# Optimization experiments

Measured on AMD Instinct MI355X. Metric: run time of the kernel, lower is better.

Reference implementation:

```python
import jax, jax.numpy as jnp
import numpy as np

B, F, H, W, C = 1, 16, 32, 32, 128


def setup_inputs() -> dict:
    key = jax.random.key(0)
    ks = jax.random.split(key, 6)
    w = lambda k: jax.random.normal(k, (C, C), jnp.float32) * 0.02
    return {
        "x": jax.random.normal(ks[0], (B, F, H, W, C), jnp.float32),
        "gamma": jnp.ones((C,), jnp.float32),
        "wq": w(ks[1]), "bq": jnp.zeros((C,), jnp.float32),
        "wk": w(ks[2]), "bk": jnp.zeros((C,), jnp.float32),
        "wv": w(ks[3]), "bv": jnp.zeros((C,), jnp.float32),
        "wo": w(ks[4]), "bo": jnp.zeros((C,), jnp.float32),
    }


def reference(x, gamma, wq, bq, wk, bk, wv, bv, wo, bo):
    b, f, h, w_, c = x.shape
    s, n_hw = f * h * w_, h * w_
    identity = x

    # RMSNorm variant: L2-normalize over channels, rescale by sqrt(C) * gamma
    xn = x / (jnp.linalg.norm(x, axis=-1, keepdims=True) + 1e-8)
    xn = xn * (c ** 0.5) * gamma

    # 1x1x1 convs == pointwise linear projections; flatten to tokens [b, s, c]
    xn = xn.reshape(b, s, c)
    q = xn @ wq + bq
    k = xn @ wk + bk
    v = xn @ wv + bv

    # frame-causal block mask: query at frame i attends to all keys in frames <= i
    frame = jnp.arange(s) // n_hw                      # [s]
    allowed = frame[:, None] >= frame[None, :]          # [s, s] bool

    scale = 1.0 / jnp.sqrt(c)
    scores = jnp.einsum('bqc,bkc->bqk', q, k) * scale   # [b, s, s]
    scores = jnp.where(allowed, scores, -jnp.inf)
    attn = jax.nn.softmax(scores, axis=-1)
    out = jnp.einsum('bqk,bkc->bqc', attn, v)           # [b, s, c]

    out = out @ wo + bo
    return out.reshape(b, f, h, w_, c) + identity
```

## Files before the change

kernel.cpp:

```cpp
#include <hip/hip_runtime.h>
#include <hip/hip_bf16.h>

typedef __bf16 bf16x8 __attribute__((ext_vector_type(8)));
typedef float f32x4 __attribute__((ext_vector_type(4)));
typedef unsigned short u16;
typedef unsigned int u32;
typedef u16 ushort8 __attribute__((ext_vector_type(8)));

#define S_TOK 16384
#define C_DIM 128
#define L2E 1.4426950408889634f
#define QK_SCALE 0.08838834764831845f
#define SQRTC 11.313708498984761f

#define NBLK 512
#define TPB 34

#define WT_OFF   0u
#define BIAS_OFF 131072u
#define XN_OFF   147456u
#define O_OFF    XN_OFF
#define Q_OFF    (XN_OFF + 4194304u)
#define K_OFF    (Q_OFF + 4194304u)
#define VT_OFF   (K_OFF + 4194304u)
#define PART_OFF (VT_OFF + 4194304u)
#define ML_OFF   (PART_OFF + 20971520u)

__device__ __forceinline__ int in_is_bf16(const void* gamma) {
  return ((const u16*)gamma)[0] == 0x3F80;
}
__device__ __forceinline__ float ldf(const void* p, int i, int bf) {
  if (bf) { u32 b = ((const u16*)p)[i]; return __uint_as_float(b << 16); }
  return ((const float*)p)[i];
}
__device__ __forceinline__ float b2f(u16 b) { return __uint_as_float((u32)b << 16); }
__device__ __forceinline__ u16 f2b(float f) {
  return __builtin_bit_cast(u16, (__bf16)f);
}
__device__ __forceinline__ void gld16(const void* g, void* l) {
  __builtin_amdgcn_global_load_lds((const __attribute__((address_space(1))) u32*)g,
                                   (__attribute__((address_space(3))) u32*)l, 16, 0, 0);
}
__device__ __forceinline__ int qb_of(int t) {
  int F = 0;
  while (64 * (F + 1) * (F + 2) <= t) F++;
  int span = 16 * (F + 1);
  return 8 * F + (t - 64 * F * (F + 1)) / span;
}
__device__ __forceinline__ int start_of(int qq) {
  int Fq = qq >> 3, iq = qq & 7;
  return 16 * (Fq + 1) * (4 * Fq + iq);
}

__global__ void prep_kernel(const void* wq, const void* bq, const void* wk, const void* bk,
                            const void* wv, const void* bv, const void* wo, const void* bo,
                            const void* gamma, char* ws) {
  int bf = in_is_bf16(gamma);
  if (blockIdx.x < 256) {
    int gid = blockIdx.x * 256 + threadIdx.x;
    int m = gid >> 14; int rem = gid & 16383;
    int k = rem >> 7; int n = rem & 127;
    const void* W = (m == 0) ? wq : (m == 1) ? wk : (m == 2) ? wv : wo;
    float v = ldf(W, rem, bf);
    if (m == 0) v *= QK_SCALE;
    *(u16*)(ws + WT_OFF + (u32)m * 32768u + (u32)n * 256u + (((u32)k * 2u) ^ (u32)((n & 7) << 4))) = f2b(v);
  } else {
    int idx = (blockIdx.x - 256) * 256 + threadIdx.x;
    if (idx < 512) {
      int m = idx >> 7; int c = idx & 127;
      const void* B = (m == 0) ? bq : (m == 1) ? bk : (m == 2) ? bv : bo;
      float v = ldf(B, c, bf);
      if (m == 0) v *= QK_SCALE;
      ((float*)(ws + BIAS_OFF))[idx] = v;
    }
  }
}

__global__ void __launch_bounds__(256) norm_kernel(const void* x, const void* gamma, char* ws) {
  int bf = in_is_bf16(gamma);
  int t = blockIdx.x * 256 + threadIdx.x;
  int tok = t >> 5; int sub = t & 31;
  int base = tok * 128 + sub * 4;
  float f[4];
  if (bf) {
    ushort4 v = ((const ushort4*)x)[base >> 2];
    f[0] = __uint_as_float((u32)v.x << 16); f[1] = __uint_as_float((u32)v.y << 16);
    f[2] = __uint_as_float((u32)v.z << 16); f[3] = __uint_as_float((u32)v.w << 16);
  } else {
    float4 v = ((const float4*)x)[base >> 2];
    f[0] = v.x; f[1] = v.y; f[2] = v.z; f[3] = v.w;
  }
  float ss = f[0]*f[0] + f[1]*f[1] + f[2]*f[2] + f[3]*f[3];
  #pragma unroll
  for (int m = 1; m < 32; m <<= 1) ss += __shfl_xor(ss, m);
  float fac = SQRTC / (sqrtf(ss) + 1e-8f);
  u16 o[4];
  #pragma unroll
  for (int j = 0; j < 4; j++) { float g = ldf(gamma, sub * 4 + j, bf); o[j] = f2b(f[j] * fac * g); }
  *(ushort4*)(ws + XN_OFF + (u32)tok * 256u + (((u32)sub * 8u) ^ (u32)((tok & 7) << 4))) =
      make_ushort4(o[0], o[1], o[2], o[3]);
}

__global__ void __launch_bounds__(256) qkv_kernel(char* ws) {
  __shared__ char lds[65536];
  int tid = threadIdx.x; int wid = tid >> 6; int lane = tid & 63;
  int blk = blockIdx.x & 127;
  int m = blockIdx.x >> 7;
  #pragma unroll
  for (int i = 0; i < 8; i++) {
    u32 seg = (u32)(i * 4 + wid) * 1024u;
    gld16(ws + XN_OFF + (u32)blk * 32768u + seg + (u32)lane * 16u, lds + seg);
    gld16(ws + WT_OFF + (u32)m * 32768u + seg + (u32)lane * 16u, lds + 32768 + seg);
  }
  __syncthreads();
  const float* bias = (const float*)(ws + BIAS_OFF);
  int rb = wid * 32;
  f32x4 acc[2][8];
  #pragma unroll
  for (int a = 0; a < 2; a++)
    #pragma unroll
    for (int b = 0; b < 8; b++) acc[a][b] = (f32x4){0.f, 0.f, 0.f, 0.f};
  #pragma unroll
  for (int kt = 0; kt < 4; kt++) {
    bf16x8 afr[2];
    #pragma unroll
    for (int mt = 0; mt < 2; mt++) {
      int row = rb + mt * 16 + (lane & 15);
      afr[mt] = *(const bf16x8*)(lds + row * 256 + ((kt * 64 + ((lane >> 4) * 16)) ^ ((row & 7) << 4)));
    }
    #pragma unroll
    for (int nt = 0; nt < 8; nt++) {
      int nr = nt * 16 + (lane & 15);
      bf16x8 bfr = *(const bf16x8*)(lds + 32768 + nr * 256 + ((kt * 64 + ((lane >> 4) * 16)) ^ ((nr & 7) << 4)));
      #pragma unroll
      for (int mt = 0; mt < 2; mt++)
        acc[mt][nt] = __builtin_amdgcn_mfma_f32_16x16x32_bf16(afr[mt], bfr, acc[mt][nt], 0, 0, 0);
    }
  }
  #pragma unroll
  for (int mt = 0; mt < 2; mt++)
    #pragma unroll
    for (int nt = 0; nt < 8; nt++) {
      int tok0 = blk * 128 + rb + mt * 16 + (lane >> 4) * 4;
      int c = (lane & 15) + nt * 16;
      float bv_ = bias[m * 128 + c];
      if (m == 0) {
        #pragma unroll
        for (int r = 0; r < 4; r++)
          *(u16*)(ws + Q_OFF + ((u32)(tok0 + r) * 128u + (u32)c) * 2u) = f2b(acc[mt][nt][r] + bv_);
      } else if (m == 1) {
        #pragma unroll
        for (int r = 0; r < 4; r++) {
          int tok = tok0 + r;
          *(u16*)(ws + K_OFF + (u32)tok * 256u + (((u32)c * 2u) ^ (u32)((tok & 7) << 4))) =
              f2b(acc[mt][nt][r] + bv_);
        }
      } else {
        u16 pk[4];
        #pragma unroll
        for (int r = 0; r < 4; r++) pk[r] = f2b(acc[mt][nt][r] + bv_);
        u32 off = (u32)c * 32768u + (u32)(tok0 & ~63) * 2u + (((u32)(tok0 & 63) * 2u) ^ (u32)((c & 7) << 4));
        *(ushort4*)(ws + VT_OFF + off) = make_ushort4(pk[0], pk[1], pk[2], pk[3]);
      }
    }
}

__global__ void __launch_bounds__(512, 4) attn_part_kernel(char* ws) {
  __shared__ char lds[65536];
  int tid = threadIdx.x; int wid = tid >> 6; int lane = tid & 63;
  int q = lane & 15; int g = lane >> 4;
  int b = blockIdx.x;
  int slot = b;
  for (int qq = 1; qq < 128; qq++) {
    int Sx = start_of(qq);
    if (Sx < TPB * b && (Sx % TPB) != 0) slot++;
  }
  u32 swzq = (u32)((q & 7) << 4);
  char* pbase = lds + 49152 + wid * 2048 + q * 128;
  ushort8 ones_u;
  #pragma unroll
  for (int e = 0; e < 8; e++) ones_u[e] = 0x3F80;
  bf16x8 ones = __builtin_bit_cast(bf16x8, ones_u);

  auto stageK = [&](int t) {
    #pragma unroll
    for (int i = 0; i < 2; i++) {
      u32 seg = (u32)(i * 8 + wid) * 1024u;
      gld16(ws + K_OFF + (u32)t * 16384u + seg + (u32)lane * 16u, lds + seg);
    }
  };
  auto stageV = [&](int t, int buf) {
    #pragma unroll
    for (int i = 0; i < 2; i++) {
      u32 seg = (u32)(i * 8 + wid) * 1024u;
      u32 gi = seg + (u32)lane * 16u;
      u32 c = gi >> 7; u32 off = gi & 127u;
      gld16(ws + VT_OFF + c * 32768u + (u32)t * 128u + off, lds + 16384 + buf * 16384 + seg);
    }
  };

  int t0 = TPB * b, remaining = TPB;
  while (remaining > 0) {
    int F = 0;
    while (64 * (F + 1) * (F + 2) <= t0) F++;
    int fb = 64 * F * (F + 1); int span = 16 * (F + 1);
    int i = (t0 - fb) / span; int l = t0 - fb - i * span;
    int qb = 8 * F + i;
    int nt = min(remaining, span - l);

    int row = qb * 128 + wid * 16 + q;
    bf16x8 aq[4];
    const char* qp = ws + Q_OFF + (u32)row * 256u + (u32)(g * 16);
    #pragma unroll
    for (int kt = 0; kt < 4; kt++) aq[kt] = *(const bf16x8*)(qp + kt * 64);
    f32x4 acc[8];
    #pragma unroll
    for (int z = 0; z < 8; z++) acc[z] = (f32x4){0.f, 0.f, 0.f, 0.f};
    f32x4 accl = (f32x4){0.f, 0.f, 0.f, 0.f};
    float m_run = -1e30f;
    float mL2 = m_run * L2E;

    __syncthreads();
    stageK(l); stageV(l, 0);
    for (int it = 0; it < nt; it++) {
      int t = l + it; int cur = it & 1;
      __syncthreads();
      if (it + 1 < nt) stageV(t + 1, cur ^ 1);
      f32x4 sfr[4];
      #pragma unroll
      for (int z = 0; z < 4; z++) sfr[z] = (f32x4){0.f, 0.f, 0.f, 0.f};
      __builtin_amdgcn_s_setprio(1);
      #pragma unroll
      for (int kt = 0; kt < 4; kt++) {
        #pragma unroll
        for (int ntk = 0; ntk < 4; ntk++) {
          int key = q + ntk * 16;
          bf16x8 bk = *(const bf16x8*)(lds + key * 256 + ((kt * 64 + g * 16) ^ ((key & 7) << 4)));
          sfr[ntk] = __builtin_amdgcn_mfma_f32_16x16x32_bf16(bk, aq[kt], sfr[ntk], 0, 0, 0);
        }
      }
      __builtin_amdgcn_s_setprio(0);
      float tm = fmaxf(fmaxf(fmaxf(sfr[0][0], sfr[0][1]), fmaxf(sfr[0][2], sfr[0][3])),
                       fmaxf(fmaxf(sfr[1][0], sfr[1][1]), fmaxf(sfr[1][2], sfr[1][3])));
      float tm2 = fmaxf(fmaxf(fmaxf(sfr[2][0], sfr[2][1]), fmaxf(sfr[2][2], sfr[2][3])),
                        fmaxf(fmaxf(sfr[3][0], sfr[3][1]), fmaxf(sfr[3][2], sfr[3][3])));
      tm = fmaxf(tm, tm2);
      tm = fmaxf(tm, __shfl_xor(tm, 16));
      tm = fmaxf(tm, __shfl_xor(tm, 32));
      if (__any(tm > m_run + 8.0f)) {
        float mnew = fmaxf(m_run, tm);
        float alpha = exp2f((m_run - mnew) * L2E);
        #pragma unroll
        for (int ct = 0; ct < 8; ct++)
          #pragma unroll
          for (int r = 0; r < 4; r++) acc[ct][r] *= alpha;
        #pragma unroll
        for (int r = 0; r < 4; r++) accl[r] *= alpha;
        m_run = mnew; mL2 = m_run * L2E;
      }
      #pragma unroll
      for (int ntk = 0; ntk < 4; ntk++) {
        float p0 = exp2f(sfr[ntk][0] * L2E - mL2);
        float p1 = exp2f(sfr[ntk][1] * L2E - mL2);
        float p2 = exp2f(sfr[ntk][2] * L2E - mL2);
        float p3 = exp2f(sfr[ntk][3] * L2E - mL2);
        u32 w0, w1;
        asm("v_cvt_pk_bf16_f32 %0, %1, %2" : "=v"(w0) : "v"(p0), "v"(p1));
        asm("v_cvt_pk_bf16_f32 %0, %1, %2" : "=v"(w1) : "v"(p2), "v"(p3));
        *(uint2*)(pbase + (((u32)(ntk * 32 + g * 8)) ^ swzq)) = make_uint2(w0, w1);
      }
      __syncthreads();
      if (it + 1 < nt) stageK(t + 1);
      const char* vbase = lds + 16384 + cur * 16384;
      __builtin_amdgcn_s_setprio(1);
      #pragma unroll
      for (int kt = 0; kt < 2; kt++) {
        bf16x8 pfr = *(const bf16x8*)(pbase + (((u32)(kt * 64 + g * 16)) ^ swzq));
        accl = __builtin_amdgcn_mfma_f32_16x16x32_bf16(ones, pfr, accl, 0, 0, 0);
        #pragma unroll
        for (int ct = 0; ct < 8; ct++) {
          int crow = q + ct * 16;
          bf16x8 va = *(const bf16x8*)(vbase + crow * 128 + ((kt * 64 + g * 16) ^ ((crow & 7) << 4)));
          acc[ct] = __builtin_amdgcn_mfma_f32_16x16x32_bf16(va, pfr, acc[ct], 0, 0, 0);
        }
      }
      __builtin_amdgcn_s_setprio(0);
    }
    float l_run = accl[0];
    float rinv = 1.0f / l_run;
    int lrow = wid * 16 + q;
    char* pb2 = ws + PART_OFF + (u32)slot * 32768u + (u32)lrow * 256u;
    #pragma unroll
    for (int ct = 0; ct < 8; ct++) {
      ushort4 pk;
      pk.x = f2b(acc[ct][0] * rinv); pk.y = f2b(acc[ct][1] * rinv);
      pk.z = f2b(acc[ct][2] * rinv); pk.w = f2b(acc[ct][3] * rinv);
      *(ushort4*)(pb2 + ct * 32 + g * 8) = pk;
    }
    if (g == 0) ((float2*)(ws + ML_OFF))[slot * 128 + lrow] = make_float2(m_run, l_run);
    t0 += nt; remaining -= nt; slot++;
  }
}

__global__ void __launch_bounds__(256) combine_kernel(char* ws) {
  int qb = blockIdx.x >> 2;
  int seg = blockIdx.x & 3;
  int Sq = start_of(qb);
  int Eq = Sq + 16 * ((qb >> 3) + 1);
  int c_lo = Sq / TPB, c_hi = (Eq - 1) / TPB;
  int bse0 = c_lo;
  for (int qq = 1; qq < 128; qq++) {
    int Sx = start_of(qq);
    if (Sx < TPB * c_lo && (Sx % TPB) != 0) bse0++;
  }
  int tid = threadIdx.x;
  int row = seg * 32 + (tid >> 3);
  int oct = tid & 7;
  const float2* ml = (const float2*)(ws + ML_OFF);
  float M = -1e30f;
  {
    int bse = bse0;
    for (int c = c_lo; c <= c_hi; c++) {
      int qbf = qb_of(TPB * c);
      int qbl = qb_of(TPB * c + TPB - 1);
      int slot = bse + (qb - qbf);
      M = fmaxf(M, ml[slot * 128 + row].x);
      bse += qbl - qbf + 1;
    }
  }
  float a[16];
  #pragma unroll
  for (int k = 0; k < 16; k++) a[k] = 0.f;
  float D = 0.f;
  {
    int bse = bse0;
    for (int c = c_lo; c <= c_hi; c++) {
      int qbf = qb_of(TPB * c);
      int qbl = qb_of(TPB * c + TPB - 1);
      int slot = bse + (qb - qbf);
      bse += qbl - qbf + 1;
      float2 m_l = ml[slot * 128 + row];
      float w = exp2f((m_l.x - M) * L2E) * m_l.y;
      D += w;
      const u16* o = (const u16*)(ws + PART_OFF + (u32)slot * 32768u + (u32)row * 256u + (u32)oct * 32u);
      ushort8 v0 = *(const ushort8*)o;
      ushort8 v1 = *(const ushort8*)(o + 8);
      #pragma unroll
      for (int e = 0; e < 8; e++) { a[e] += w * b2f(v0[e]); a[8 + e] += w * b2f(v1[e]); }
    }
  }
  float Dinv = 1.0f / D;
  int grow = qb * 128 + row;
  ushort8 w0, w1;
  #pragma unroll
  for (int e = 0; e < 8; e++) { w0[e] = f2b(a[e] * Dinv); w1[e] = f2b(a[8 + e] * Dinv); }
  u32 rbase = (u32)grow * 256u;
  u32 swz = (u32)((row & 7) << 4);
  *(ushort8*)(ws + O_OFF + rbase + (((u32)oct * 32u) ^ swz)) = w0;
  *(ushort8*)(ws + O_OFF + rbase + (((u32)oct * 32u + 16u) ^ swz)) = w1;
}

__global__ void __launch_bounds__(256) out_kernel(const void* x, const void* gamma, char* ws, void* out) {
  __shared__ char lds[49152];
  int bf = in_is_bf16(gamma);
  int tid = threadIdx.x; int wid = tid >> 6; int lane = tid & 63;
  int g = lane >> 4;
  int blk = blockIdx.x;
  #pragma unroll
  for (int i = 0; i < 4; i++) {
    u32 seg = (u32)(i * 4 + wid) * 1024u;
    gld16(ws + O_OFF + (u32)blk * 16384u + seg + (u32)lane * 16u, lds + seg);
  }
  #pragma unroll
  for (int i = 0; i < 8; i++) {
    u32 seg = (u32)(i * 4 + wid) * 1024u;
    gld16(ws + WT_OFF + 3u * 32768u + seg + (u32)lane * 16u, lds + 16384 + seg);
  }
  __syncthreads();
  f32x4 acc[8];
  #pragma unroll
  for (int z = 0; z < 8; z++) acc[z] = (f32x4){0.f, 0.f, 0.f, 0.f};
  int rb = wid * 16;
  #pragma unroll
  for (int kt = 0; kt < 4; kt++) {
    int row = rb + (lane & 15);
    bf16x8 afr = *(const bf16x8*)(lds + row * 256 + ((kt * 64 + g * 16) ^ ((row & 7) << 4)));
    #pragma unroll
    for (int nt = 0; nt < 8; nt++) {
      int nr = nt * 16 + (lane & 15);
      bf16x8 bfr = *(const bf16x8*)(lds + 16384 + nr * 256 + ((kt * 64 + g * 16) ^ ((nr & 7) << 4)));
      acc[nt] = __builtin_amdgcn_mfma_f32_16x16x32_bf16(afr, bfr, acc[nt], 0, 0, 0);
    }
  }
  const float* bias = (const float*)(ws + BIAS_OFF) + 3 * 128;
  #pragma unroll
  for (int nt = 0; nt < 8; nt++) {
    int c = (lane & 15) + nt * 16;
    float bv_ = bias[c];
    #pragma unroll
    for (int r = 0; r < 4; r++) {
      int tok = blk * 64 + rb + g * 4 + r;
      float v = acc[nt][r] + bv_ + ldf(x, tok * 128 + c, bf);
      if (bf) ((u16*)out)[tok * 128 + c] = f2b(v);
      else    ((float*)out)[tok * 128 + c] = v;
    }
  }
}

extern "C" void kernel_launch(void* const* d_in, const int* in_sizes, int n_in,
                              void* d_out, int out_size, void* d_ws, size_t ws_size,
                              hipStream_t stream) {
  (void)in_sizes; (void)n_in; (void)out_size; (void)ws_size;
  const void* x     = d_in[0];
  const void* gamma = d_in[1];
  const void* wq = d_in[2]; const void* bq = d_in[3];
  const void* wk = d_in[4]; const void* bk = d_in[5];
  const void* wv = d_in[6]; const void* bv = d_in[7];
  const void* wo = d_in[8]; const void* bo = d_in[9];
  char* ws = (char*)d_ws;
  hipLaunchKernelGGL(prep_kernel, dim3(258), dim3(256), 0, stream,
                     wq, bq, wk, bk, wv, bv, wo, bo, gamma, ws);
  hipLaunchKernelGGL(norm_kernel, dim3(2048), dim3(256), 0, stream, x, gamma, ws);
  hipLaunchKernelGGL(qkv_kernel, dim3(384), dim3(256), 0, stream, ws);
  hipLaunchKernelGGL(attn_part_kernel, dim3(NBLK), dim3(512), 0, stream, ws);
  hipLaunchKernelGGL(combine_kernel, dim3(512), dim3(256), 0, stream, ws);
  hipLaunchKernelGGL(out_kernel, dim3(256), dim3(256), 0, stream, x, gamma, ws, d_out);
}
```

Before: 185.9 us.

## Pre-fragment K/V layouts, double query rows per wave, merge prep and norm kernels

The QKV kernel now writes K and V directly in MFMA-fragment order, so the attention kernel stages them with contiguous per-thread loads and reads operands with lane-linear LDS accesses instead of swizzled addressing. The attention kernel drops to 4 waves per block, each wave handling 32 query rows (two 16-row tiles), so every K/V fragment read from LDS feeds two MFMAs. Weight/bias prep is folded into the norm kernel to save a launch, and the output projection processes 128 tokens per block. The trade-off is higher register pressure per wave and fewer waves per block, which may reduce latency hiding.

```diff
diff --git a/kernel.cpp b/kernel.cpp
--- a/kernel.cpp
+++ b/kernel.cpp
@@ -22,8 +22,8 @@
 #define O_OFF    XN_OFF
 #define Q_OFF    (XN_OFF + 4194304u)
 #define K_OFF    (Q_OFF + 4194304u)
-#define VT_OFF   (K_OFF + 4194304u)
-#define PART_OFF (VT_OFF + 4194304u)
+#define VF_OFF   (K_OFF + 4194304u)
+#define PART_OFF (VF_OFF + 4194304u)
 #define ML_OFF   (PART_OFF + 20971520u)
 
 __device__ __forceinline__ int in_is_bf16(const void* gamma) {
@@ -52,32 +52,32 @@
   return 16 * (Fq + 1) * (4 * Fq + iq);
 }
 
-__global__ void prep_kernel(const void* wq, const void* bq, const void* wk, const void* bk,
-                            const void* wv, const void* bv, const void* wo, const void* bo,
-                            const void* gamma, char* ws) {
+__global__ void __launch_bounds__(256) prep_norm_kernel(const void* x, const void* gamma,
+    const void* wq, const void* bq, const void* wk, const void* bk,
+    const void* wv, const void* bv, const void* wo, const void* bo, char* ws) {
   int bf = in_is_bf16(gamma);
-  if (blockIdx.x < 256) {
-    int gid = blockIdx.x * 256 + threadIdx.x;
-    int m = gid >> 14; int rem = gid & 16383;
-    int k = rem >> 7; int n = rem & 127;
-    const void* W = (m == 0) ? wq : (m == 1) ? wk : (m == 2) ? wv : wo;
-    float v = ldf(W, rem, bf);
-    if (m == 0) v *= QK_SCALE;
-    *(u16*)(ws + WT_OFF + (u32)m * 32768u + (u32)n * 256u + (((u32)k * 2u) ^ (u32)((n & 7) << 4))) = f2b(v);
-  } else {
-    int idx = (blockIdx.x - 256) * 256 + threadIdx.x;
-    if (idx < 512) {
-      int m = idx >> 7; int c = idx & 127;
-      const void* B = (m == 0) ? bq : (m == 1) ? bk : (m == 2) ? bv : bo;
-      float v = ldf(B, c, bf);
+  if (blockIdx.x >= 2048) {
+    int bb = blockIdx.x - 2048;
+    if (bb < 256) {
+      int gid = bb * 256 + threadIdx.x;
+      int m = gid >> 14; int rem = gid & 16383;
+      int k = rem >> 7; int n = rem & 127;
+      const void* W = (m == 0) ? wq : (m == 1) ? wk : (m == 2) ? wv : wo;
+      float v = ldf(W, rem, bf);
       if (m == 0) v *= QK_SCALE;
-      ((float*)(ws + BIAS_OFF))[idx] = v;
-    }
-  }
-}
-
-__global__ void __launch_bounds__(256) norm_kernel(const void* x, const void* gamma, char* ws) {
-  int bf = in_is_bf16(gamma);
+      *(u16*)(ws + WT_OFF + (u32)m * 32768u + (u32)n * 256u + (((u32)k * 2u) ^ (u32)((n & 7) << 4))) = f2b(v);
+    } else {
+      int idx = (bb - 256) * 256 + threadIdx.x;
+      if (idx < 512) {
+        int m = idx >> 7; int c = idx & 127;
+        const void* B = (m == 0) ? bq : (m == 1) ? bk : (m == 2) ? bv : bo;
+        float v = ldf(B, c, bf);
+        if (m == 0) v *= QK_SCALE;
+        ((float*)(ws + BIAS_OFF))[idx] = v;
+      }
+    }
+    return;
+  }
   int t = blockIdx.x * 256 + threadIdx.x;
   int tok = t >> 5; int sub = t & 31;
   int base = tok * 128 + sub * 4;
@@ -149,23 +149,25 @@
         for (int r = 0; r < 4; r++)
           *(u16*)(ws + Q_OFF + ((u32)(tok0 + r) * 128u + (u32)c) * 2u) = f2b(acc[mt][nt][r] + bv_);
       } else if (m == 1) {
-        #pragma unroll
-        for (int r = 0; r < 4; r++) {
-          int tok = tok0 + r;
-          *(u16*)(ws + K_OFF + (u32)tok * 256u + (((u32)c * 2u) ^ (u32)((tok & 7) << 4))) =
-              f2b(acc[mt][nt][r] + bv_);
-        }
+        int ktc = c >> 5, gc = (c >> 3) & 3, jc = c & 7;
+        int tile = tok0 >> 6, ntk = (tok0 >> 4) & 3, qv0 = tok0 & 15;
+        char* bp = ws + K_OFF + (u32)tile * 16384u + (u32)(ktc * 4 + ntk) * 1024u + (u32)(16 * gc) * 16u + (u32)jc * 2u;
+        #pragma unroll
+        for (int r = 0; r < 4; r++)
+          *(u16*)(bp + (u32)(qv0 + r) * 16u) = f2b(acc[mt][nt][r] + bv_);
       } else {
+        int tile = tok0 >> 6, kts = (tok0 >> 5) & 1, gv = (tok0 >> 3) & 3, j0 = tok0 & 7;
+        int ctv = c >> 4, qv2 = c & 15;
         u16 pk[4];
         #pragma unroll
         for (int r = 0; r < 4; r++) pk[r] = f2b(acc[mt][nt][r] + bv_);
-        u32 off = (u32)c * 32768u + (u32)(tok0 & ~63) * 2u + (((u32)(tok0 & 63) * 2u) ^ (u32)((c & 7) << 4));
-        *(ushort4*)(ws + VT_OFF + off) = make_ushort4(pk[0], pk[1], pk[2], pk[3]);
-      }
-    }
-}
-
-__global__ void __launch_bounds__(512, 4) attn_part_kernel(char* ws) {
+        *(ushort4*)(ws + VF_OFF + (u32)tile * 16384u + (u32)(kts * 8 + ctv) * 1024u
+                    + (u32)(qv2 + 16 * gv) * 16u + (u32)j0 * 2u) = make_ushort4(pk[0], pk[1], pk[2], pk[3]);
+      }
+    }
+}
+
+__global__ void __launch_bounds__(256, 2) attn_part_kernel(char* ws) {
   __shared__ char lds[65536];
   int tid = threadIdx.x; int wid = tid >> 6; int lane = tid & 63;
   int q = lane & 15; int g = lane >> 4;
@@ -175,8 +177,7 @@
     int Sx = start_of(qq);
     if (Sx < TPB * b && (Sx % TPB) != 0) slot++;
   }
-  u32 swzq = (u32)((q & 7) << 4);
-  char* pbase = lds + 49152 + wid * 2048 + q * 128;
+  char* pbase = lds + 49152 + wid * 4096;
   ushort8 ones_u;
   #pragma unroll
   for (int e = 0; e < 8; e++) ones_u[e] = 0x3F80;
@@ -184,18 +185,16 @@
 
   auto stageK = [&](int t) {
     #pragma unroll
-    for (int i = 0; i < 2; i++) {
-      u32 seg = (u32)(i * 8 + wid) * 1024u;
-      gld16(ws + K_OFF + (u32)t * 16384u + seg + (u32)lane * 16u, lds + seg);
+    for (int i = 0; i < 4; i++) {
+      u32 off = (u32)(i * 4096) + (u32)tid * 16u;
+      gld16(ws + K_OFF + (u32)t * 16384u + off, lds + off);
     }
   };
   auto stageV = [&](int t, int buf) {
     #pragma unroll
-    for (int i = 0; i < 2; i++) {
-      u32 seg = (u32)(i * 8 + wid) * 1024u;
-      u32 gi = seg + (u32)lane * 16u;
-      u32 c = gi >> 7; u32 off = gi & 127u;
-      gld16(ws + VT_OFF + c * 32768u + (u32)t * 128u + off, lds + 16384 + buf * 16384 + seg);
+    for (int i = 0; i < 4; i++) {
+      u32 off = (u32)(i * 4096) + (u32)tid * 16u;
+      gld16(ws + VF_OFF + (u32)t * 16384u + off, lds + 16384 + buf * 16384 + off);
     }
   };
 
@@ -208,17 +207,21 @@
     int qb = 8 * F + i;
     int nt = min(remaining, span - l);
 
-    int row = qb * 128 + wid * 16 + q;
-    bf16x8 aq[4];
-    const char* qp = ws + Q_OFF + (u32)row * 256u + (u32)(g * 16);
-    #pragma unroll
-    for (int kt = 0; kt < 4; kt++) aq[kt] = *(const bf16x8*)(qp + kt * 64);
-    f32x4 acc[8];
-    #pragma unroll
-    for (int z = 0; z < 8; z++) acc[z] = (f32x4){0.f, 0.f, 0.f, 0.f};
-    f32x4 accl = (f32x4){0.f, 0.f, 0.f, 0.f};
-    float m_run = -1e30f;
-    float mL2 = m_run * L2E;
+    bf16x8 aq0[4], aq1[4];
+    {
+      const char* qp0 = ws + Q_OFF + (u32)(qb * 128 + wid * 32 + q) * 256u + (u32)(g * 16);
+      #pragma unroll
+      for (int kt = 0; kt < 4; kt++) {
+        aq0[kt] = *(const bf16x8*)(qp0 + kt * 64);
+        aq1[kt] = *(const bf16x8*)(qp0 + 4096 + kt * 64);
+      }
+    }
+    f32x4 acc0[8], acc1[8];
+    #pragma unroll
+    for (int z = 0; z < 8; z++) { acc0[z] = (f32x4){0.f,0.f,0.f,0.f}; acc1[z] = (f32x4){0.f,0.f,0.f,0.f}; }
+    f32x4 accl0 = (f32x4){0.f,0.f,0.f,0.f}, accl1 = (f32x4){0.f,0.f,0.f,0.f};
+    float m0 = -1e30f, m1 = -1e30f;
+    float mL0 = m0 * L2E, mL1 = m1 * L2E;
 
     __syncthreads();
     stageK(l); stageV(l, 0);
@@ -226,78 +229,104 @@
       int t = l + it; int cur = it & 1;
       __syncthreads();
       if (it + 1 < nt) stageV(t + 1, cur ^ 1);
-      f32x4 sfr[4];
-      #pragma unroll
-      for (int z = 0; z < 4; z++) sfr[z] = (f32x4){0.f, 0.f, 0.f, 0.f};
+      f32x4 sfr0[4], sfr1[4];
+      #pragma unroll
+      for (int z = 0; z < 4; z++) { sfr0[z] = (f32x4){0.f,0.f,0.f,0.f}; sfr1[z] = (f32x4){0.f,0.f,0.f,0.f}; }
       __builtin_amdgcn_s_setprio(1);
       #pragma unroll
       for (int kt = 0; kt < 4; kt++) {
         #pragma unroll
         for (int ntk = 0; ntk < 4; ntk++) {
-          int key = q + ntk * 16;
-          bf16x8 bk = *(const bf16x8*)(lds + key * 256 + ((kt * 64 + g * 16) ^ ((key & 7) << 4)));
-          sfr[ntk] = __builtin_amdgcn_mfma_f32_16x16x32_bf16(bk, aq[kt], sfr[ntk], 0, 0, 0);
+          bf16x8 bk = *(const bf16x8*)(lds + (kt * 4 + ntk) * 1024 + (u32)lane * 16u);
+          sfr0[ntk] = __builtin_amdgcn_mfma_f32_16x16x32_bf16(bk, aq0[kt], sfr0[ntk], 0, 0, 0);
+          sfr1[ntk] = __builtin_amdgcn_mfma_f32_16x16x32_bf16(bk, aq1[kt], sfr1[ntk], 0, 0, 0);
         }
       }
       __builtin_amdgcn_s_setprio(0);
-      float tm = fmaxf(fmaxf(fmaxf(sfr[0][0], sfr[0][1]), fmaxf(sfr[0][2], sfr[0][3])),
-                       fmaxf(fmaxf(sfr[1][0], sfr[1][1]), fmaxf(sfr[1][2], sfr[1][3])));
-      float tm2 = fmaxf(fmaxf(fmaxf(sfr[2][0], sfr[2][1]), fmaxf(sfr[2][2], sfr[2][3])),
-                        fmaxf(fmaxf(sfr[3][0], sfr[3][1]), fmaxf(sfr[3][2], sfr[3][3])));
-      tm = fmaxf(tm, tm2);
-      tm = fmaxf(tm, __shfl_xor(tm, 16));
-      tm = fmaxf(tm, __shfl_xor(tm, 32));
-      if (__any(tm > m_run + 8.0f)) {
-        float mnew = fmaxf(m_run, tm);
-        float alpha = exp2f((m_run - mnew) * L2E);
+      float tm0 = fmaxf(fmaxf(fmaxf(sfr0[0][0], sfr0[0][1]), fmaxf(sfr0[0][2], sfr0[0][3])),
+                        fmaxf(fmaxf(sfr0[1][0], sfr0[1][1]), fmaxf(sfr0[1][2], sfr0[1][3])));
+      tm0 = fmaxf(tm0, fmaxf(fmaxf(fmaxf(sfr0[2][0], sfr0[2][1]), fmaxf(sfr0[2][2], sfr0[2][3])),
+                             fmaxf(fmaxf(sfr0[3][0], sfr0[3][1]), fmaxf(sfr0[3][2], sfr0[3][3]))));
+      float tm1 = fmaxf(fmaxf(fmaxf(sfr1[0][0], sfr1[0][1]), fmaxf(sfr1[0][2], sfr1[0][3])),
+                        fmaxf(fmaxf(sfr1[1][0], sfr1[1][1]), fmaxf(sfr1[1][2], sfr1[1][3])));
+      tm1 = fmaxf(tm1, fmaxf(fmaxf(fmaxf(sfr1[2][0], sfr1[2][1]), fmaxf(sfr1[2][2], sfr1[2][3])),
+                             fmaxf(fmaxf(sfr1[3][0], sfr1[3][1]), fmaxf(sfr1[3][2], sfr1[3][3]))));
+      tm0 = fmaxf(tm0, __shfl_xor(tm0, 16)); tm0 = fmaxf(tm0, __shfl_xor(tm0, 32));
+      tm1 = fmaxf(tm1, __shfl_xor(tm1, 16)); tm1 = fmaxf(tm1, __shfl_xor(tm1, 32));
+      bool need = (tm0 > m0 + 8.0f) || (tm1 > m1 + 8.0f);
+      if (__any(need)) {
+        float mn0 = fmaxf(m0, tm0), mn1 = fmaxf(m1, tm1);
+        float a0 = exp2f((m0 - mn0) * L2E), a1 = exp2f((m1 - mn1) * L2E);
         #pragma unroll
         for (int ct = 0; ct < 8; ct++)
           #pragma unroll
-          for (int r = 0; r < 4; r++) acc[ct][r] *= alpha;
-        #pragma unroll
-        for (int r = 0; r < 4; r++) accl[r] *= alpha;
-        m_run = mnew; mL2 = m_run * L2E;
+          for (int r = 0; r < 4; r++) { acc0[ct][r] *= a0; acc1[ct][r] *= a1; }
+        #pragma unroll
+        for (int r = 0; r < 4; r++) { accl0[r] *= a0; accl1[r] *= a1; }
+        m0 = mn0; m1 = mn1; mL0 = m0 * L2E; mL1 = m1 * L2E;
       }
       #pragma unroll
       for (int ntk = 0; ntk < 4; ntk++) {
-        float p0 = exp2f(sfr[ntk][0] * L2E - mL2);
-        float p1 = exp2f(sfr[ntk][1] * L2E - mL2);
-        float p2 = exp2f(sfr[ntk][2] * L2E - mL2);
-        float p3 = exp2f(sfr[ntk][3] * L2E - mL2);
-        u32 w0, w1;
-        asm("v_cvt_pk_bf16_f32 %0, %1, %2" : "=v"(w0) : "v"(p0), "v"(p1));
-        asm("v_cvt_pk_bf16_f32 %0, %1, %2" : "=v"(w1) : "v"(p2), "v"(p3));
-        *(uint2*)(pbase + (((u32)(ntk * 32 + g * 8)) ^ swzq)) = make_uint2(w0, w1);
+        u32 dl = (u32)(q + 16 * (((ntk & 1) << 1) | (g >> 1))) * 16u + (u32)((g & 1) * 8);
+        {
+          float p0 = exp2f(__builtin_fmaf(sfr0[ntk][0], L2E, -mL0));
+          float p1 = exp2f(__builtin_fmaf(sfr0[ntk][1], L2E, -mL0));
+          float p2 = exp2f(__builtin_fmaf(sfr0[ntk][2], L2E, -mL0));
+          float p3 = exp2f(__builtin_fmaf(sfr0[ntk][3], L2E, -mL0));
+          u32 w0, w1;
+          asm("v_cvt_pk_bf16_f32 %0, %1, %2" : "=v"(w0) : "v"(p0), "v"(p1));
+          asm("v_cvt_pk_bf16_f32 %0, %1, %2" : "=v"(w1) : "v"(p2), "v"(p3));
+          *(uint2*)(pbase + ((ntk >> 1) * 2 + 0) * 1024 + dl) = make_uint2(w0, w1);
+        }
+        {
+          float p0 = exp2f(__builtin_fmaf(sfr1[ntk][0], L2E, -mL1));
+          float p1 = exp2f(__builtin_fmaf(sfr1[ntk][1], L2E, -mL1));
+          float p2 = exp2f(__builtin_fmaf(sfr1[ntk][2], L2E, -mL1));
+          float p3 = exp2f(__builtin_fmaf(sfr1[ntk][3], L2E, -mL1));
+          u32 w0, w1;
+          asm("v_cvt_pk_bf16_f32 %0, %1, %2" : "=v"(w0) : "v"(p0), "v"(p1));
+          asm("v_cvt_pk_bf16_f32 %0, %1, %2" : "=v"(w1) : "v"(p2), "v"(p3));
+          *(uint2*)(pbase + ((ntk >> 1) * 2 + 1) * 1024 + dl) = make_uint2(w0, w1);
+        }
       }
       __syncthreads();
       if (it + 1 < nt) stageK(t + 1);
-      const char* vbase = lds + 16384 + cur * 16384;
+      const char* vb = lds + 16384 + cur * 16384;
       __builtin_amdgcn_s_setprio(1);
       #pragma unroll
-      for (int kt = 0; kt < 2; kt++) {
-        bf16x8 pfr = *(const bf16x8*)(pbase + (((u32)(kt * 64 + g * 16)) ^ swzq));
-        accl = __builtin_amdgcn_mfma_f32_16x16x32_bf16(ones, pfr, accl, 0, 0, 0);
+      for (int kts = 0; kts < 2; kts++) {
+        bf16x8 pf0 = *(const bf16x8*)(pbase + (kts * 2 + 0) * 1024 + (u32)lane * 16u);
+        bf16x8 pf1 = *(const bf16x8*)(pbase + (kts * 2 + 1) * 1024 + (u32)lane * 16u);
+        accl0 = __builtin_amdgcn_mfma_f32_16x16x32_bf16(ones, pf0, accl0, 0, 0, 0);
+        accl1 = __builtin_amdgcn_mfma_f32_16x16x32_bf16(ones, pf1, accl1, 0, 0, 0);
         #pragma unroll
         for (int ct = 0; ct < 8; ct++) {
-          int crow = q + ct * 16;
-          bf16x8 va = *(const bf16x8*)(vbase + crow * 128 + ((kt * 64 + g * 16) ^ ((crow & 7) << 4)));
-          acc[ct] = __builtin_amdgcn_mfma_f32_16x16x32_bf16(va, pfr, acc[ct], 0, 0, 0);
+          bf16x8 va = *(const bf16x8*)(vb + (kts * 8 + ct) * 1024 + (u32)lane * 16u);
+          acc0[ct] = __builtin_amdgcn_mfma_f32_16x16x32_bf16(va, pf0, acc0[ct], 0, 0, 0);
+          acc1[ct] = __builtin_amdgcn_mfma_f32_16x16x32_bf16(va, pf1, acc1[ct], 0, 0, 0);
         }
       }
       __builtin_amdgcn_s_setprio(0);
     }
-    float l_run = accl[0];
-    float rinv = 1.0f / l_run;
-    int lrow = wid * 16 + q;
-    char* pb2 = ws + PART_OFF + (u32)slot * 32768u + (u32)lrow * 256u;
+    float l0 = accl0[0], l1 = accl1[0];
+    float ri0 = 1.0f / l0, ri1 = 1.0f / l1;
+    int lrow0 = wid * 32 + q;
+    char* pb2 = ws + PART_OFF + (u32)slot * 32768u + (u32)lrow0 * 256u;
     #pragma unroll
     for (int ct = 0; ct < 8; ct++) {
       ushort4 pk;
-      pk.x = f2b(acc[ct][0] * rinv); pk.y = f2b(acc[ct][1] * rinv);
-      pk.z = f2b(acc[ct][2] * rinv); pk.w = f2b(acc[ct][3] * rinv);
+      pk.x = f2b(acc0[ct][0] * ri0); pk.y = f2b(acc0[ct][1] * ri0);
+      pk.z = f2b(acc0[ct][2] * ri0); pk.w = f2b(acc0[ct][3] * ri0);
       *(ushort4*)(pb2 + ct * 32 + g * 8) = pk;
-    }
-    if (g == 0) ((float2*)(ws + ML_OFF))[slot * 128 + lrow] = make_float2(m_run, l_run);
+      ushort4 pk1;
+      pk1.x = f2b(acc1[ct][0] * ri1); pk1.y = f2b(acc1[ct][1] * ri1);
+      pk1.z = f2b(acc1[ct][2] * ri1); pk1.w = f2b(acc1[ct][3] * ri1);
+      *(ushort4*)(pb2 + 16 * 256 + ct * 32 + g * 8) = pk1;
+    }
+    if (g == 0) {
+      ((float2*)(ws + ML_OFF))[slot * 128 + lrow0] = make_float2(m0, l0);
+      ((float2*)(ws + ML_OFF))[slot * 128 + lrow0 + 16] = make_float2(m1, l1);
+    }
     t0 += nt; remaining -= nt; slot++;
   }
 }
@@ -361,50 +390,55 @@
 }
 
 __global__ void __launch_bounds__(256) out_kernel(const void* x, const void* gamma, char* ws, void* out) {
-  __shared__ char lds[49152];
+  __shared__ char lds[65536];
   int bf = in_is_bf16(gamma);
   int tid = threadIdx.x; int wid = tid >> 6; int lane = tid & 63;
-  int g = lane >> 4;
   int blk = blockIdx.x;
-  #pragma unroll
-  for (int i = 0; i < 4; i++) {
-    u32 seg = (u32)(i * 4 + wid) * 1024u;
-    gld16(ws + O_OFF + (u32)blk * 16384u + seg + (u32)lane * 16u, lds + seg);
-  }
   #pragma unroll
   for (int i = 0; i < 8; i++) {
     u32 seg = (u32)(i * 4 + wid) * 1024u;
-    gld16(ws + WT_OFF + 3u * 32768u + seg + (u32)lane * 16u, lds + 16384 + seg);
+    gld16(ws + O_OFF + (u32)blk * 32768u + seg + (u32)lane * 16u, lds + seg);
+    gld16(ws + WT_OFF + 3u * 32768u + seg + (u32)lane * 16u, lds + 32768 + seg);
   }
   __syncthreads();
-  f32x4 acc[8];
-  #pragma unroll
-  for (int z = 0; z < 8; z++) acc[z] = (f32x4){0.f, 0.f, 0.f, 0.f};
-  int rb = wid * 16;
+  f32x4 acc[2][8];
+  #pragma unroll
+  for (int a = 0; a < 2; a++)
+    #pragma unroll
+    for (int b = 0; b < 8; b++) acc[a][b] = (f32x4){0.f, 0.f, 0.f, 0.f};
+  int rb = wid * 32;
   #pragma unroll
   for (int kt = 0; kt < 4; kt++) {
-    int row = rb + (lane & 15);
-    bf16x8 afr = *(const bf16x8*)(lds + row * 256 + ((kt * 64 + g * 16) ^ ((row & 7) << 4)));
+    bf16x8 afr[2];
+    #pragma unroll
+    for (int mt = 0; mt < 2; mt++) {
+      int row = rb + mt * 16 + (lane & 15);
+      afr[mt] = *(const bf16x8*)(lds + row * 256 + ((kt * 64 + ((lane >> 4) * 16)) ^ ((row & 7) << 4)));
+    }
     #pragma unroll
     for (int nt = 0; nt < 8; nt++) {
       int nr = nt * 16 + (lane & 15);
-      bf16x8 bfr = *(const bf16x8*)(lds + 16384 + nr * 256 + ((kt * 64 + g * 16) ^ ((nr & 7) << 4)));
-      acc[nt] = __builtin_amdgcn_mfma_f32_16x16x32_bf16(afr, bfr, acc[nt], 0, 0, 0);
+      bf16x8 bfr = *(const bf16x8*)(lds + 32768 + nr * 256 + ((kt * 64 + ((lane >> 4) * 16)) ^ ((nr & 7) << 4)));
+      #pragma unroll
+      for (int mt = 0; mt < 2; mt++)
+        acc[mt][nt] = __builtin_amdgcn_mfma_f32_16x16x32_bf16(afr[mt], bfr, acc[mt][nt], 0, 0, 0);
     }
   }
   const float* bias = (const float*)(ws + BIAS_OFF) + 3 * 128;
   #pragma unroll
-  for (int nt = 0; nt < 8; nt++) {
-    int c = (lane & 15) + nt * 16;
-    float bv_ = bias[c];
-    #pragma unroll
-    for (int r = 0; r < 4; r++) {
-      int tok = blk * 64 + rb + g * 4 + r;
-      float v = acc[nt][r] + bv_ + ldf(x, tok * 128 + c, bf);
-      if (bf) ((u16*)out)[tok * 128 + c] = f2b(v);
-      else    ((float*)out)[tok * 128 + c] = v;
-    }
-  }
+  for (int mt = 0; mt < 2; mt++)
+    #pragma unroll
+    for (int nt = 0; nt < 8; nt++) {
+      int c = (lane & 15) + nt * 16;
+      float bv_ = bias[c];
+      #pragma unroll
+      for (int r = 0; r < 4; r++) {
+        int tok = blk * 128 + rb + mt * 16 + (lane >> 4) * 4 + r;
+        float v = acc[mt][nt][r] + bv_ + ldf(x, tok * 128 + c, bf);
+        if (bf) ((u16*)out)[tok * 128 + c] = f2b(v);
+        else    ((float*)out)[tok * 128 + c] = v;
+      }
+    }
 }
 
 extern "C" void kernel_launch(void* const* d_in, const int* in_sizes, int n_in,
@@ -418,11 +452,10 @@
   const void* wv = d_in[6]; const void* bv = d_in[7];
   const void* wo = d_in[8]; const void* bo = d_in[9];
   char* ws = (char*)d_ws;
-  hipLaunchKernelGGL(prep_kernel, dim3(258), dim3(256), 0, stream,
-                     wq, bq, wk, bk, wv, bv, wo, bo, gamma, ws);
-  hipLaunchKernelGGL(norm_kernel, dim3(2048), dim3(256), 0, stream, x, gamma, ws);
+  hipLaunchKernelGGL(prep_norm_kernel, dim3(2306), dim3(256), 0, stream,
+                     x, gamma, wq, bq, wk, bk, wv, bv, wo, bo, ws);
   hipLaunchKernelGGL(qkv_kernel, dim3(384), dim3(256), 0, stream, ws);
-  hipLaunchKernelGGL(attn_part_kernel, dim3(NBLK), dim3(512), 0, stream, ws);
+  hipLaunchKernelGGL(attn_part_kernel, dim3(NBLK), dim3(256), 0, stream, ws);
   hipLaunchKernelGGL(combine_kernel, dim3(512), dim3(256), 0, stream, ws);
-  hipLaunchKernelGGL(out_kernel, dim3(256), dim3(256), 0, stream, x, gamma, ws, d_out);
-}
+  hipLaunchKernelGGL(out_kernel, dim3(128), dim3(256), 0, stream, x, gamma, ws, d_out);
+}
```

After: 176.6 us. 1.05x faster.
